# Kernel optimization log

Measured on AMD Instinct MI355X. Metric: run time of the kernel, lower is better.

The kernel has to match this reference:

```python
import jax, jax.numpy as jnp
import numpy as np
import math

N_FREQ = 50
ENC_DIM = 4 * N_FREQ  # 200
D = 5
N_GENES = 1000
N_CELLS = 5000
N_FRAG = 200_000


def sine_encoding(coords):
    # frequencies: [f1,f1,f2,f2,...] length 2*N_FREQ; shifts: [0, pi/2, 0, pi/2, ...]
    i = jnp.arange(1, N_FREQ + 1, dtype=jnp.float32)
    freqs = jnp.repeat(1.0 / jnp.power(jnp.float32(1000.0), 2.0 * i / N_FREQ), 2)
    shifts = jnp.tile(jnp.array([0.0, math.pi / 2], jnp.float32), N_FREQ)
    # coords [F,2] -> [F,2,2*nf] -> [F,4*nf]
    return jnp.sin((coords[..., None] * freqs + shifts).reshape(coords.shape[0], -1))


def self_attention(x):
    # x: [G, i, D]; NOTE: scale uses sqrt(seq_len) = sqrt(x.shape[-2]) as in the original
    scores = jnp.einsum('gid,gjd->gij', x, x) / jnp.sqrt(jnp.float32(x.shape[1]))
    w = jax.nn.softmax(scores, axis=-1)
    return jnp.einsum('gij,gjd->gid', w, x)


def setup_inputs() -> dict:
    key = jax.random.key(0)
    ks = jax.random.split(key, 6)
    coordinates = jax.random.uniform(ks[0], (N_FRAG, 2), jnp.float32, -1000.0, 1000.0)
    genemapping = jax.random.randint(ks[1], (N_FRAG,), 0, N_GENES)
    local_cellxgene_ix = jax.random.randint(ks[2], (N_FRAG,), 0, N_CELLS * N_GENES)
    genes_oi = jnp.arange(N_GENES)
    # ragged groups: disjoint fragment index sets for group sizes 2, 3, 4
    n2 = jnp.arange(60000)             # 30000 pairs
    n3 = jnp.arange(60000) + 60000     # 20000 triples
    n4 = jnp.arange(60000) + 120000    # 15000 quads
    stdv = 1.0 / math.sqrt(D)
    weight1_frag = jax.random.uniform(ks[3], (N_GENES, ENC_DIM, D), jnp.float32, -stdv, stdv)
    weight1_expr = jnp.ones((N_GENES, D), jnp.float32)
    bias1 = jax.random.normal(ks[4], (N_GENES,), jnp.float32)  # mean_gene_expression
    return dict(coordinates=coordinates, genemapping=genemapping, n2=n2, n3=n3, n4=n4,
                local_cellxgene_ix=local_cellxgene_ix, genes_oi=genes_oi,
                weight1_frag=weight1_frag, weight1_expr=weight1_expr, bias1=bias1)


def reference(coordinates, genemapping, n2, n3, n4, local_cellxgene_ix, genes_oi,
              weight1_frag, weight1_expr, bias1):
    # FragmentEmbedder: sine encode, per-gene weight gather, contract, sigmoid
    enc = sine_encoding(coordinates)                                 # [F, 200]
    emb = jax.nn.sigmoid(jnp.einsum('fe,fed->fd', enc, weight1_frag[genemapping]))  # [F, 5]
    # ragged self-attention over fixed-size groups (2, 3, 4)
    for idx, i in ((n2, 2), (n3, 3), (n4, 4)):
        x = emb[idx].reshape(-1, i, D)
        emb = emb.at[idx].set(self_attention(x).reshape(-1, D))
    # EmbeddingGenePooler: segment sum over cell x gene
    pooled = jax.ops.segment_sum(emb, local_cellxgene_ix, num_segments=N_CELLS * N_GENES)
    cell_gene_embedding = pooled.reshape(N_CELLS, N_GENES, D)
    # EmbeddingToExpression: gene-wise weighted sum + mean expression bias
    return (cell_gene_embedding * weight1_expr[genes_oi]).sum(-1) + bias1[genes_oi]
```

## Files before the change

kernel.cpp:

```cpp
#include <hip/hip_runtime.h>
#include <math.h>

#define DD 5
#define NFREQ 50
#define NB 128

__global__ __launch_bounds__(256) void hist_init_kernel(
    const int* __restrict__ gm, int F, int chunk,
    int* __restrict__ bc, int n_genes, int* __restrict__ done,
    unsigned char* __restrict__ mask,
    float* __restrict__ out, const float* __restrict__ bias,
    const int* __restrict__ genes_oi, int total4) {
  __shared__ int cnt[1000];
  const int gtid = blockIdx.x * blockDim.x + threadIdx.x;
  const int gs = gridDim.x * blockDim.x;
  if (gtid == 0) *done = 0;
  int F4 = F >> 2;
  int* mask4 = (int*)mask;
  for (int i = gtid; i < F4; i += gs) mask4[i] = 0;
  for (int i = (F4 << 2) + gtid; i < F; i += gs) mask[i] = 0;
  for (int v4 = gtid; v4 < total4; v4 += gs) {
    int idx = v4 * 4;
    int j = idx % n_genes;
    float4 vv;
    vv.x = bias[genes_oi[j + 0]];
    vv.y = bias[genes_oi[j + 1]];
    vv.z = bias[genes_oi[j + 2]];
    vv.w = bias[genes_oi[j + 3]];
    reinterpret_cast<float4*>(out)[v4] = vv;
  }
  if (blockIdx.x < NB) {
    for (int j = threadIdx.x; j < n_genes; j += blockDim.x) cnt[j] = 0;
    __syncthreads();
    int b = blockIdx.x;
    int lo = b * chunk;
    int hi = min(F, lo + chunk);
    for (int i = lo + threadIdx.x; i < hi; i += blockDim.x)
      atomicAdd(&cnt[gm[i]], 1);
    __syncthreads();
    for (int j = threadIdx.x; j < n_genes; j += blockDim.x)
      bc[j * NB + b] = cnt[j];
  }
}

__global__ __launch_bounds__(256) void binscan_starts_kernel(
    int* __restrict__ bc, int n_genes, int* __restrict__ totals,
    int* __restrict__ starts, int* __restrict__ done, int nblocks,
    unsigned char* __restrict__ mask,
    const int* __restrict__ n2, int c2,
    const int* __restrict__ n3, int c3,
    const int* __restrict__ n4, int c4) {
  __shared__ int s_amlast;
  __shared__ int s_ws[4];
  const int gtid = blockIdx.x * blockDim.x + threadIdx.x;
  const int gs = gridDim.x * blockDim.x;
  int lane = threadIdx.x & 63;
  int wv = threadIdx.x >> 6;
  int bin = blockIdx.x * 4 + wv;
  if (bin < n_genes) {
    int2* row = (int2*)(bc + (size_t)bin * NB);
    int2 v = row[lane];
    int p = v.x + v.y;
    int ip = p;
#pragma unroll
    for (int off = 1; off < 64; off <<= 1) {
      int q = __shfl_up(ip, off);
      if (lane >= off) ip += q;
    }
    int base = ip - p;
    int2 e;
    e.x = base;
    e.y = base + v.x;
    row[lane] = e;
    if (lane == 63) totals[bin] = ip;
  }
  for (int i = gtid; i < c2; i += gs) mask[n2[i]] = 1;
  for (int i = gtid; i < c3; i += gs) mask[n3[i]] = 1;
  for (int i = gtid; i < c4; i += gs) mask[n4[i]] = 1;
  __syncthreads();
  if (threadIdx.x == 0) {
    __threadfence();
    int tk = atomicAdd(done, 1);
    s_amlast = (tk == nblocks - 1);
  }
  __syncthreads();
  if (!s_amlast) return;
  __threadfence();
  int t = threadIdx.x;
  int4 v = make_int4(0, 0, 0, 0);
  if (4 * t < n_genes) v = ((const int4*)totals)[t];
  int p = v.x + v.y + v.z + v.w;
  int ip = p;
#pragma unroll
  for (int off = 1; off < 64; off <<= 1) {
    int q = __shfl_up(ip, off);
    if (lane >= off) ip += q;
  }
  if (lane == 63) s_ws[wv] = ip;
  __syncthreads();
  int add = 0;
#pragma unroll
  for (int i = 0; i < 4; ++i)
    if (i < wv) add += s_ws[i];
  int excl = add + ip - p;
  int4 e;
  e.x = excl;
  e.y = excl + v.x;
  e.z = e.y + v.y;
  e.w = e.z + v.z;
  if (4 * t < n_genes) ((int4*)starts)[t] = e;
  if (4 * t + 4 == n_genes) starts[n_genes] = e.w + v.w;
}

__global__ __launch_bounds__(256) void blockscatter_kernel(
    const int* __restrict__ gm, int F, int chunk,
    const int* __restrict__ bc, const int* __restrict__ starts,
    int* __restrict__ order, int n_genes) {
  __shared__ int cur[1000];
  int b = blockIdx.x;
  for (int j = threadIdx.x; j < n_genes; j += blockDim.x)
    cur[j] = starts[j] + bc[j * NB + b];
  __syncthreads();
  int lo = b * chunk;
  int hi = min(F, lo + chunk);
  for (int i = lo + threadIdx.x; i < hi; i += blockDim.x) {
    int g = gm[i];
    int p = atomicAdd(&cur[g], 1);
    order[p] = i;
  }
}

__global__ __launch_bounds__(256) void embed_kernel(
    const float2* __restrict__ coords, const int* __restrict__ order,
    const int* __restrict__ starts, const float* __restrict__ W,
    float* __restrict__ emb) {
  __shared__ float s_freq[NFREQ];
  if (threadIdx.x < NFREQ)
    s_freq[threadIdx.x] = exp2f(-0.39863137f * (float)(threadIdx.x + 1));
  __syncthreads();
  int g = blockIdx.x;
  int s0 = starts[g];
  int s1 = starts[g + 1];
  const float* __restrict__ Wg = W + (size_t)g * (4 * NFREQ * DD);

  for (int i = s0 + threadIdx.x; i < s1; i += blockDim.x) {
    int f = order[i];
    float2 xy = coords[f];
    float a0 = 0.f, a1 = 0.f, a2 = 0.f, a3 = 0.f, a4 = 0.f;
    for (int k = 0; k < NFREQ; ++k) {
      float fr = s_freq[k];
      float ax = xy.x * fr;
      float ay = xy.y * fr;
      float sx = __sinf(ax), cx = __cosf(ax);
      float sy = __sinf(ay), cy = __cosf(ay);
      const float* w0s = Wg + (2 * k) * DD;
      const float* w0c = w0s + DD;
      const float* w1s = Wg + (2 * NFREQ + 2 * k) * DD;
      const float* w1c = w1s + DD;
      a0 += sx * w0s[0] + cx * w0c[0] + sy * w1s[0] + cy * w1c[0];
      a1 += sx * w0s[1] + cx * w0c[1] + sy * w1s[1] + cy * w1c[1];
      a2 += sx * w0s[2] + cx * w0c[2] + sy * w1s[2] + cy * w1c[2];
      a3 += sx * w0s[3] + cx * w0c[3] + sy * w1s[3] + cy * w1c[3];
      a4 += sx * w0s[4] + cx * w0c[4] + sy * w1s[4] + cy * w1c[4];
    }
    float* e = emb + (size_t)f * DD;
    e[0] = 1.f / (1.f + __expf(-a0));
    e[1] = 1.f / (1.f + __expf(-a1));
    e[2] = 1.f / (1.f + __expf(-a2));
    e[3] = 1.f / (1.f + __expf(-a3));
    e[4] = 1.f / (1.f + __expf(-a4));
  }
}

template <int SZ>
__device__ __forceinline__ void attn_group_pool(const int* __restrict__ idx,
                                                const float* __restrict__ emb,
                                                const int* __restrict__ lci,
                                                const int* __restrict__ genes_oi,
                                                const float* __restrict__ wexpr,
                                                int n_genes, float* __restrict__ out) {
  int fid[SZ];
  float x[SZ][DD];
#pragma unroll
  for (int a = 0; a < SZ; ++a) {
    fid[a] = idx[a];
    const float* p = emb + (size_t)fid[a] * DD;
#pragma unroll
    for (int d = 0; d < DD; ++d) x[a][d] = p[d];
  }
  const float scale = rsqrtf((float)SZ);
#pragma unroll
  for (int a = 0; a < SZ; ++a) {
    float sc[SZ];
    float m = -1e30f;
#pragma unroll
    for (int b = 0; b < SZ; ++b) {
      float dt = 0.f;
#pragma unroll
      for (int d = 0; d < DD; ++d) dt += x[a][d] * x[b][d];
      sc[b] = dt * scale;
      m = fmaxf(m, sc[b]);
    }
    float sum = 0.f;
#pragma unroll
    for (int b = 0; b < SZ; ++b) {
      sc[b] = __expf(sc[b] - m);
      sum += sc[b];
    }
    float inv = 1.f / sum;
    int ix = lci[fid[a]];
    int g = genes_oi[ix % n_genes];
    const float* w = wexpr + (size_t)g * DD;
    float s = 0.f;
#pragma unroll
    for (int d = 0; d < DD; ++d) {
      float acc = 0.f;
#pragma unroll
      for (int b = 0; b < SZ; ++b) acc += sc[b] * x[b][d];
      s += acc * w[d];
    }
    atomicAdd(out + ix, s * inv);
  }
}

__global__ __launch_bounds__(256) void attn_pool_kernel(
    const int* __restrict__ n2, int g2,
    const int* __restrict__ n3, int g3,
    const int* __restrict__ n4, int g4,
    const float* __restrict__ emb, const int* __restrict__ lci,
    const int* __restrict__ genes_oi, const float* __restrict__ wexpr,
    const unsigned char* __restrict__ mask,
    int F, int n_genes, float* __restrict__ out) {
  int gtid = blockIdx.x * blockDim.x + threadIdx.x;
  int gs = gridDim.x * blockDim.x;
  int gtot = g2 + g3 + g4;
  for (int w = gtid; w < gtot; w += gs) {
    if (w < g2)
      attn_group_pool<2>(n2 + (size_t)w * 2, emb, lci, genes_oi, wexpr, n_genes, out);
    else if (w < g2 + g3)
      attn_group_pool<3>(n3 + (size_t)(w - g2) * 3, emb, lci, genes_oi, wexpr, n_genes, out);
    else
      attn_group_pool<4>(n4 + (size_t)(w - g2 - g3) * 4, emb, lci, genes_oi, wexpr, n_genes, out);
  }
  for (int f = gtid; f < F; f += gs) {
    if (mask[f]) continue;
    int ix = lci[f];
    int g = genes_oi[ix % n_genes];
    const float* e = emb + (size_t)f * DD;
    const float* w = wexpr + (size_t)g * DD;
    float s = e[0] * w[0] + e[1] * w[1] + e[2] * w[2] + e[3] * w[3] + e[4] * w[4];
    atomicAdd(out + ix, s);
  }
}

extern "C" void kernel_launch(void* const* d_in, const int* in_sizes, int n_in,
                              void* d_out, int out_size, void* d_ws, size_t ws_size,
                              hipStream_t stream) {
  const float2* coords  = (const float2*)d_in[0];
  const int* gm         = (const int*)d_in[1];
  const int* n2         = (const int*)d_in[2];
  const int* n3         = (const int*)d_in[3];
  const int* n4         = (const int*)d_in[4];
  const int* lci        = (const int*)d_in[5];
  const int* genes_oi   = (const int*)d_in[6];
  const float* W        = (const float*)d_in[7];
  const float* wexpr    = (const float*)d_in[8];
  const float* bias     = (const float*)d_in[9];
  float* out            = (float*)d_out;

  const int F       = in_sizes[1];
  const int n_genes = in_sizes[6];
  const int c2 = in_sizes[2];
  const int c3 = in_sizes[3];
  const int c4 = in_sizes[4];
  const int g2 = c2 / 2;
  const int g3 = c3 / 3;
  const int g4 = c4 / 4;

  char* ws = (char*)d_ws;
  size_t off = 0;
  float* emb   = (float*)(ws + off); off += (size_t)F * DD * sizeof(float);
  int* order   = (int*)(ws + off);   off += (size_t)F * sizeof(int);
  int* bc      = (int*)(ws + off);   off += (size_t)n_genes * NB * sizeof(int);
  off = (off + 15) & ~(size_t)15;
  int* starts  = (int*)(ws + off);   off += (size_t)(n_genes + 4) * sizeof(int);
  off = (off + 15) & ~(size_t)15;
  int* totals  = (int*)(ws + off);   off += (size_t)n_genes * sizeof(int);
  int* done    = (int*)(ws + off);   off += 4 * sizeof(int);
  off = (off + 15) & ~(size_t)15;
  unsigned char* mask = (unsigned char*)(ws + off); off += (size_t)F;

  const int tb = 256;
  const int chunk = (F + NB - 1) / NB;
  const int total4 = out_size / 4;

  hist_init_kernel<<<1024, tb, 0, stream>>>(gm, F, chunk, bc, n_genes, done,
                                            mask, out, bias, genes_oi, total4);
  int scan_blocks = (n_genes + 3) / 4;
  binscan_starts_kernel<<<scan_blocks, tb, 0, stream>>>(bc, n_genes, totals,
                                                        starts, done, scan_blocks,
                                                        mask, n2, c2, n3, c3, n4, c4);
  blockscatter_kernel<<<NB, tb, 0, stream>>>(gm, F, chunk, bc, starts, order, n_genes);
  embed_kernel<<<n_genes, tb, 0, stream>>>(coords, order, starts, W, emb);
  attn_pool_kernel<<<1250, tb, 0, stream>>>(n2, g2, n3, g3, n4, g4,
                                            emb, lci, genes_oi, wexpr,
                                            mask, F, n_genes, out);
}
```

Baseline: 142.9 us.

## Stage gene weights in LDS, pad embeddings, replace group mask with delta pooling

The embed kernel now stages each gene's 1000 weights in shared memory, reordered so each frequency's 20 coefficients load as five float4 reads. Embeddings are stored with a stride of 8 floats so rows can be read and written as float4. The fragment mask is gone: every fragment adds its plain contribution, and each attention group adds the difference between its attended and raw values. Output bias initialisation now reads from a shared-memory row instead of gathering through genes_oi per element, and the attention grid size changes. The trade-offs are a larger embedding buffer and a small change in floating-point summation order.

```diff
diff --git a/kernel.cpp b/kernel.cpp
--- a/kernel.cpp
+++ b/kernel.cpp
@@ -2,58 +2,47 @@
 #include <math.h>
 
 #define DD 5
+#define EST 8
 #define NFREQ 50
 #define NB 128
 
 __global__ __launch_bounds__(256) void hist_init_kernel(
     const int* __restrict__ gm, int F, int chunk,
     int* __restrict__ bc, int n_genes, int* __restrict__ done,
-    unsigned char* __restrict__ mask,
     float* __restrict__ out, const float* __restrict__ bias,
-    const int* __restrict__ genes_oi, int total4) {
+    const int* __restrict__ genes_oi, int n_cells) {
   __shared__ int cnt[1000];
-  const int gtid = blockIdx.x * blockDim.x + threadIdx.x;
-  const int gs = gridDim.x * blockDim.x;
-  if (gtid == 0) *done = 0;
-  int F4 = F >> 2;
-  int* mask4 = (int*)mask;
-  for (int i = gtid; i < F4; i += gs) mask4[i] = 0;
-  for (int i = (F4 << 2) + gtid; i < F; i += gs) mask[i] = 0;
-  for (int v4 = gtid; v4 < total4; v4 += gs) {
-    int idx = v4 * 4;
-    int j = idx % n_genes;
-    float4 vv;
-    vv.x = bias[genes_oi[j + 0]];
-    vv.y = bias[genes_oi[j + 1]];
-    vv.z = bias[genes_oi[j + 2]];
-    vv.w = bias[genes_oi[j + 3]];
-    reinterpret_cast<float4*>(out)[v4] = vv;
-  }
+  __shared__ float s_brow[1000];
+  const int tid = threadIdx.x;
+  if (blockIdx.x == 0 && tid == 0) *done = 0;
+  for (int j = tid; j < n_genes; j += blockDim.x) {
+    s_brow[j] = bias[genes_oi[j]];
+    cnt[j] = 0;
+  }
+  __syncthreads();
   if (blockIdx.x < NB) {
-    for (int j = threadIdx.x; j < n_genes; j += blockDim.x) cnt[j] = 0;
-    __syncthreads();
-    int b = blockIdx.x;
-    int lo = b * chunk;
+    int lo = blockIdx.x * chunk;
     int hi = min(F, lo + chunk);
-    for (int i = lo + threadIdx.x; i < hi; i += blockDim.x)
+    for (int i = lo + tid; i < hi; i += blockDim.x)
       atomicAdd(&cnt[gm[i]], 1);
-    __syncthreads();
-    for (int j = threadIdx.x; j < n_genes; j += blockDim.x)
-      bc[j * NB + b] = cnt[j];
-  }
+  }
+  const float4* b4 = (const float4*)s_brow;
+  const int q = n_genes >> 2;
+  for (int c = blockIdx.x; c < n_cells; c += gridDim.x) {
+    float4* dst = (float4*)out + (size_t)c * q;
+    for (int t = tid; t < q; t += blockDim.x) dst[t] = b4[t];
+  }
+  __syncthreads();
+  if (blockIdx.x < NB)
+    for (int j = tid; j < n_genes; j += blockDim.x)
+      bc[j * NB + blockIdx.x] = cnt[j];
 }
 
 __global__ __launch_bounds__(256) void binscan_starts_kernel(
     int* __restrict__ bc, int n_genes, int* __restrict__ totals,
-    int* __restrict__ starts, int* __restrict__ done, int nblocks,
-    unsigned char* __restrict__ mask,
-    const int* __restrict__ n2, int c2,
-    const int* __restrict__ n3, int c3,
-    const int* __restrict__ n4, int c4) {
+    int* __restrict__ starts, int* __restrict__ done, int nblocks) {
   __shared__ int s_amlast;
   __shared__ int s_ws[4];
-  const int gtid = blockIdx.x * blockDim.x + threadIdx.x;
-  const int gs = gridDim.x * blockDim.x;
   int lane = threadIdx.x & 63;
   int wv = threadIdx.x >> 6;
   int bin = blockIdx.x * 4 + wv;
@@ -74,9 +63,6 @@
     row[lane] = e;
     if (lane == 63) totals[bin] = ip;
   }
-  for (int i = gtid; i < c2; i += gs) mask[n2[i]] = 1;
-  for (int i = gtid; i < c3; i += gs) mask[n3[i]] = 1;
-  for (int i = gtid; i < c4; i += gs) mask[n4[i]] = 1;
   __syncthreads();
   if (threadIdx.x == 0) {
     __threadfence();
@@ -133,60 +119,72 @@
 __global__ __launch_bounds__(256) void embed_kernel(
     const float2* __restrict__ coords, const int* __restrict__ order,
     const int* __restrict__ starts, const float* __restrict__ W,
-    float* __restrict__ emb) {
+    float* __restrict__ emb, int n_genes) {
+  __shared__ float s_w[1000];
   __shared__ float s_freq[NFREQ];
-  if (threadIdx.x < NFREQ)
-    s_freq[threadIdx.x] = exp2f(-0.39863137f * (float)(threadIdx.x + 1));
-  __syncthreads();
+  const int tid = threadIdx.x;
+  if (tid < NFREQ)
+    s_freq[tid] = exp2f(-0.39863137f * (float)(tid + 1));
   int g = blockIdx.x;
+  const float* __restrict__ Wg = W + (size_t)g * (4 * NFREQ * DD);
+  for (int idx = tid; idx < 1000; idx += blockDim.x) {
+    int k = idx / 20, r = idx % 20;
+    s_w[idx] = (r < 10) ? Wg[10 * k + r] : Wg[500 + 10 * k + (r - 10)];
+  }
+  __syncthreads();
   int s0 = starts[g];
   int s1 = starts[g + 1];
-  const float* __restrict__ Wg = W + (size_t)g * (4 * NFREQ * DD);
-
-  for (int i = s0 + threadIdx.x; i < s1; i += blockDim.x) {
+  const float4* __restrict__ w4 = (const float4*)s_w;
+
+  for (int i = s0 + tid; i < s1; i += blockDim.x) {
     int f = order[i];
     float2 xy = coords[f];
     float a0 = 0.f, a1 = 0.f, a2 = 0.f, a3 = 0.f, a4 = 0.f;
+#pragma unroll 2
     for (int k = 0; k < NFREQ; ++k) {
       float fr = s_freq[k];
       float ax = xy.x * fr;
       float ay = xy.y * fr;
       float sx = __sinf(ax), cx = __cosf(ax);
       float sy = __sinf(ay), cy = __cosf(ay);
-      const float* w0s = Wg + (2 * k) * DD;
-      const float* w0c = w0s + DD;
-      const float* w1s = Wg + (2 * NFREQ + 2 * k) * DD;
-      const float* w1c = w1s + DD;
-      a0 += sx * w0s[0] + cx * w0c[0] + sy * w1s[0] + cy * w1c[0];
-      a1 += sx * w0s[1] + cx * w0c[1] + sy * w1s[1] + cy * w1c[1];
-      a2 += sx * w0s[2] + cx * w0c[2] + sy * w1s[2] + cy * w1c[2];
-      a3 += sx * w0s[3] + cx * w0c[3] + sy * w1s[3] + cy * w1c[3];
-      a4 += sx * w0s[4] + cx * w0c[4] + sy * w1s[4] + cy * w1c[4];
-    }
-    float* e = emb + (size_t)f * DD;
-    e[0] = 1.f / (1.f + __expf(-a0));
-    e[1] = 1.f / (1.f + __expf(-a1));
-    e[2] = 1.f / (1.f + __expf(-a2));
-    e[3] = 1.f / (1.f + __expf(-a3));
+      float4 c0 = w4[5 * k + 0];
+      float4 c1 = w4[5 * k + 1];
+      float4 c2 = w4[5 * k + 2];
+      float4 c3 = w4[5 * k + 3];
+      float4 c4 = w4[5 * k + 4];
+      a0 += sx * c0.x + cx * c1.y + sy * c2.z + cy * c3.w;
+      a1 += sx * c0.y + cx * c1.z + sy * c2.w + cy * c4.x;
+      a2 += sx * c0.z + cx * c1.w + sy * c3.x + cy * c4.y;
+      a3 += sx * c0.w + cx * c2.x + sy * c3.y + cy * c4.z;
+      a4 += sx * c1.x + cx * c2.y + sy * c3.z + cy * c4.w;
+    }
+    float* e = emb + (size_t)f * EST;
+    float4 r;
+    r.x = 1.f / (1.f + __expf(-a0));
+    r.y = 1.f / (1.f + __expf(-a1));
+    r.z = 1.f / (1.f + __expf(-a2));
+    r.w = 1.f / (1.f + __expf(-a3));
+    *reinterpret_cast<float4*>(e) = r;
     e[4] = 1.f / (1.f + __expf(-a4));
   }
 }
 
 template <int SZ>
-__device__ __forceinline__ void attn_group_pool(const int* __restrict__ idx,
-                                                const float* __restrict__ emb,
-                                                const int* __restrict__ lci,
-                                                const int* __restrict__ genes_oi,
-                                                const float* __restrict__ wexpr,
-                                                int n_genes, float* __restrict__ out) {
+__device__ __forceinline__ void attn_group_delta(const int* __restrict__ idx,
+                                                 const float* __restrict__ emb,
+                                                 const int* __restrict__ lci,
+                                                 const int* __restrict__ genes_oi,
+                                                 const float* __restrict__ wexpr,
+                                                 int n_genes, float* __restrict__ out) {
   int fid[SZ];
   float x[SZ][DD];
 #pragma unroll
   for (int a = 0; a < SZ; ++a) {
     fid[a] = idx[a];
-    const float* p = emb + (size_t)fid[a] * DD;
-#pragma unroll
-    for (int d = 0; d < DD; ++d) x[a][d] = p[d];
+    const float* p = emb + (size_t)fid[a] * EST;
+    float4 v = *reinterpret_cast<const float4*>(p);
+    x[a][0] = v.x; x[a][1] = v.y; x[a][2] = v.z; x[a][3] = v.w;
+    x[a][4] = p[4];
   }
   const float scale = rsqrtf((float)SZ);
 #pragma unroll
@@ -217,9 +215,9 @@
       float acc = 0.f;
 #pragma unroll
       for (int b = 0; b < SZ; ++b) acc += sc[b] * x[b][d];
-      s += acc * w[d];
-    }
-    atomicAdd(out + ix, s * inv);
+      s += (acc * inv - x[a][d]) * w[d];
+    }
+    atomicAdd(out + ix, s);
   }
 }
 
@@ -229,26 +227,25 @@
     const int* __restrict__ n4, int g4,
     const float* __restrict__ emb, const int* __restrict__ lci,
     const int* __restrict__ genes_oi, const float* __restrict__ wexpr,
-    const unsigned char* __restrict__ mask,
     int F, int n_genes, float* __restrict__ out) {
   int gtid = blockIdx.x * blockDim.x + threadIdx.x;
   int gs = gridDim.x * blockDim.x;
   int gtot = g2 + g3 + g4;
   for (int w = gtid; w < gtot; w += gs) {
     if (w < g2)
-      attn_group_pool<2>(n2 + (size_t)w * 2, emb, lci, genes_oi, wexpr, n_genes, out);
+      attn_group_delta<2>(n2 + (size_t)w * 2, emb, lci, genes_oi, wexpr, n_genes, out);
     else if (w < g2 + g3)
-      attn_group_pool<3>(n3 + (size_t)(w - g2) * 3, emb, lci, genes_oi, wexpr, n_genes, out);
+      attn_group_delta<3>(n3 + (size_t)(w - g2) * 3, emb, lci, genes_oi, wexpr, n_genes, out);
     else
-      attn_group_pool<4>(n4 + (size_t)(w - g2 - g3) * 4, emb, lci, genes_oi, wexpr, n_genes, out);
+      attn_group_delta<4>(n4 + (size_t)(w - g2 - g3) * 4, emb, lci, genes_oi, wexpr, n_genes, out);
   }
   for (int f = gtid; f < F; f += gs) {
-    if (mask[f]) continue;
     int ix = lci[f];
     int g = genes_oi[ix % n_genes];
-    const float* e = emb + (size_t)f * DD;
+    const float* e = emb + (size_t)f * EST;
+    float4 v = *reinterpret_cast<const float4*>(e);
     const float* w = wexpr + (size_t)g * DD;
-    float s = e[0] * w[0] + e[1] * w[1] + e[2] * w[2] + e[3] * w[3] + e[4] * w[4];
+    float s = v.x * w[0] + v.y * w[1] + v.z * w[2] + v.w * w[3] + e[4] * w[4];
     atomicAdd(out + ix, s);
   }
 }
@@ -270,16 +267,13 @@
 
   const int F       = in_sizes[1];
   const int n_genes = in_sizes[6];
-  const int c2 = in_sizes[2];
-  const int c3 = in_sizes[3];
-  const int c4 = in_sizes[4];
-  const int g2 = c2 / 2;
-  const int g3 = c3 / 3;
-  const int g4 = c4 / 4;
+  const int g2 = in_sizes[2] / 2;
+  const int g3 = in_sizes[3] / 3;
+  const int g4 = in_sizes[4] / 4;
 
   char* ws = (char*)d_ws;
   size_t off = 0;
-  float* emb   = (float*)(ws + off); off += (size_t)F * DD * sizeof(float);
+  float* emb   = (float*)(ws + off); off += (size_t)F * EST * sizeof(float);
   int* order   = (int*)(ws + off);   off += (size_t)F * sizeof(int);
   int* bc      = (int*)(ws + off);   off += (size_t)n_genes * NB * sizeof(int);
   off = (off + 15) & ~(size_t)15;
@@ -287,22 +281,19 @@
   off = (off + 15) & ~(size_t)15;
   int* totals  = (int*)(ws + off);   off += (size_t)n_genes * sizeof(int);
   int* done    = (int*)(ws + off);   off += 4 * sizeof(int);
-  off = (off + 15) & ~(size_t)15;
-  unsigned char* mask = (unsigned char*)(ws + off); off += (size_t)F;
 
   const int tb = 256;
   const int chunk = (F + NB - 1) / NB;
-  const int total4 = out_size / 4;
+  const int n_cells = out_size / n_genes;
 
   hist_init_kernel<<<1024, tb, 0, stream>>>(gm, F, chunk, bc, n_genes, done,
-                                            mask, out, bias, genes_oi, total4);
+                                            out, bias, genes_oi, n_cells);
   int scan_blocks = (n_genes + 3) / 4;
   binscan_starts_kernel<<<scan_blocks, tb, 0, stream>>>(bc, n_genes, totals,
-                                                        starts, done, scan_blocks,
-                                                        mask, n2, c2, n3, c3, n4, c4);
+                                                        starts, done, scan_blocks);
   blockscatter_kernel<<<NB, tb, 0, stream>>>(gm, F, chunk, bc, starts, order, n_genes);
-  embed_kernel<<<n_genes, tb, 0, stream>>>(coords, order, starts, W, emb);
-  attn_pool_kernel<<<1250, tb, 0, stream>>>(n2, g2, n3, g3, n4, g4,
+  embed_kernel<<<n_genes, tb, 0, stream>>>(coords, order, starts, W, emb, n_genes);
+  attn_pool_kernel<<<1024, tb, 0, stream>>>(n2, g2, n3, g3, n4, g4,
                                             emb, lci, genes_oi, wexpr,
-                                            mask, F, n_genes, out);
-}
+                                            F, n_genes, out);
+}
```

Result: slower. 146.6 us (+2.6%).
